# Optimization experiments

Hardware: AMD Instinct MI355X
Metric: run time of the kernel (lower is better)

Reference implementation:

```python
import jax, jax.numpy as jnp
import numpy as np

N, M, C = 4096, 1024, 64
KERNEL_SIZE = (0.1, 0.1)  # box extents; threshold is kernel_size/2 on |dx|,|dy|


def setup_inputs() -> dict:
    key = jax.random.key(0)
    k1, k2, k3 = jax.random.split(key, 3)
    values = jax.random.normal(k1, (N, C), dtype=jnp.float32)
    coords = jax.random.uniform(k2, (N, 2), dtype=jnp.float32)
    query_coords = jax.random.uniform(k3, (M, 2), dtype=jnp.float32)
    return {"values": values, "coords": coords, "query_coords": query_coords}


def reference(values, coords, query_coords):
    # shift buffer is (0,0) so no shift branch; box-kernel mask branch.
    kw, kh = KERNEL_SIZE
    diffs = query_coords[:, None, :] - coords[None, :, :]          # [M, N, 2]
    mask = (jnp.abs(diffs[..., 0]) < kw / 2) & (jnp.abs(diffs[..., 1]) < kh / 2)  # [M, N]
    neg = jnp.finfo(values.dtype).min
    # per-query masked max over points == ragged split + per-segment max in the original
    masked = jnp.where(mask[:, :, None], values[None, :, :], neg)  # [M, N, C]
    return jnp.max(masked, axis=1)                                  # [M, C]
```

## Files before the change

kernel.cpp:

```cpp
#include <hip/hip_runtime.h>

constexpr int N = 4096;
constexpr int M = 1024;
constexpr int C = 64;
#define HALF_KW 0.05f
#define NEG_INF (-3.402823466e38f)

__global__ __launch_bounds__(256) void maxpool_box_kernel(
    const float* __restrict__ values,
    const float* __restrict__ coords,
    const float* __restrict__ qcoords,
    float* __restrict__ out)
{
    __shared__ int    s_cnt;
    __shared__ int    s_list[N];
    __shared__ float4 s_part[16][16];

    const int q    = blockIdx.x;
    const int tid  = threadIdx.x;
    const int lane = tid & 63;
    const int w    = tid >> 6;

    if (tid == 0) s_cnt = 0;
    __syncthreads();

    const float qx = qcoords[2 * q + 0];
    const float qy = qcoords[2 * q + 1];

    const float4* c4p = (const float4*)coords;
    #pragma unroll
    for (int i = 0; i < N / (256 * 2); ++i) {
        const int pair = i * 256 + tid;
        const float4 cc = c4p[pair];
        const bool in0 = (fabsf(qx - cc.x) < HALF_KW) && (fabsf(qy - cc.y) < HALF_KW);
        const bool in1 = (fabsf(qx - cc.z) < HALF_KW) && (fabsf(qy - cc.w) < HALF_KW);
        if (in0) { int k = atomicAdd(&s_cnt, 1); s_list[k] = 2 * pair; }
        if (in1) { int k = atomicAdd(&s_cnt, 1); s_list[k] = 2 * pair + 1; }
    }
    __syncthreads();

    const int cnt = s_cnt;
    const int G   = (cnt + 3) >> 2;
    if (cnt > 0 && tid < G * 4 - cnt) s_list[cnt + tid] = s_list[0];
    __syncthreads();

    const int sub = lane >> 4;
    const int cq  = lane & 15;
    const float4* v4 = (const float4*)values;
    float4 acc = make_float4(NEG_INF, NEG_INF, NEG_INF, NEG_INF);
    for (int g = w; g < G; g += 4) {
        const int p = s_list[g * 4 + sub];
        const float4 v = v4[p * 16 + cq];
        acc.x = fmaxf(acc.x, v.x);
        acc.y = fmaxf(acc.y, v.y);
        acc.z = fmaxf(acc.z, v.z);
        acc.w = fmaxf(acc.w, v.w);
    }
    s_part[w * 4 + sub][cq] = acc;
    __syncthreads();

    if (tid < 16) {
        float4 r = s_part[0][tid];
        #pragma unroll
        for (int k = 1; k < 16; ++k) {
            const float4 t = s_part[k][tid];
            r.x = fmaxf(r.x, t.x);
            r.y = fmaxf(r.y, t.y);
            r.z = fmaxf(r.z, t.z);
            r.w = fmaxf(r.w, t.w);
        }
        ((float4*)out)[q * 16 + tid] = r;
    }
}

extern "C" void kernel_launch(void* const* d_in, const int* in_sizes, int n_in,
                              void* d_out, int out_size, void* d_ws, size_t ws_size,
                              hipStream_t stream) {
    const float* values  = (const float*)d_in[0];
    const float* coords  = (const float*)d_in[1];
    const float* qcoords = (const float*)d_in[2];
    float* out = (float*)d_out;

    maxpool_box_kernel<<<M, 256, 0, stream>>>(values, coords, qcoords, out);
}
```

Baseline: 61.25 us.

## Bin points into a uniform grid so queries scan only nearby cells

```diff
diff --git a/kernel.cpp b/kernel.cpp
--- a/kernel.cpp
+++ b/kernel.cpp
@@ -3,13 +3,73 @@
 constexpr int N = 4096;
 constexpr int M = 1024;
 constexpr int C = 64;
+constexpr int GRID = 20;
+constexpr int NCELL = GRID * GRID;
+#define CELL_INV 20.0f
 #define HALF_KW 0.05f
 #define NEG_INF (-3.402823466e38f)
 
-__global__ __launch_bounds__(256) void maxpool_box_kernel(
+
+__global__ __launch_bounds__(1024) void bin_points_kernel(
+    const float* __restrict__ coords,
+    int* __restrict__ cell_start,
+    int* __restrict__ binned_idx,
+    float2* __restrict__ binned_xy)
+{
+    __shared__ int s_cnt[NCELL];
+    __shared__ int s_scan[512];
+    __shared__ int s_cur[NCELL];
+
+    const int tid = threadIdx.x;
+
+    if (tid < NCELL) s_cnt[tid] = 0;
+    __syncthreads();
+
+    const float4* c4 = (const float4*)coords;
+    const float4 a = c4[2 * tid];
+    const float4 b = c4[2 * tid + 1];
+    const float px[4] = {a.x, a.z, b.x, b.z};
+    const float py[4] = {a.y, a.w, b.y, b.w};
+    int cell[4];
+    #pragma unroll
+    for (int k = 0; k < 4; ++k) {
+        const int cx = min(GRID - 1, (int)(px[k] * CELL_INV));
+        const int cy = min(GRID - 1, (int)(py[k] * CELL_INV));
+        cell[k] = cy * GRID + cx;
+        atomicAdd(&s_cnt[cell[k]], 1);
+    }
+    __syncthreads();
+
+    if (tid < 512) s_scan[tid] = (tid < NCELL) ? s_cnt[tid] : 0;
+    __syncthreads();
+    for (int off = 1; off < 512; off <<= 1) {
+        int v = 0;
+        if (tid < 512) { v = s_scan[tid]; if (tid >= off) v += s_scan[tid - off]; }
+        __syncthreads();
+        if (tid < 512) s_scan[tid] = v;
+        __syncthreads();
+    }
+    if (tid <= NCELL) {
+        const int e = (tid == 0) ? 0 : s_scan[tid - 1];
+        cell_start[tid] = e;
+        if (tid < NCELL) s_cur[tid] = e;
+    }
+    __syncthreads();
+
+    #pragma unroll
+    for (int k = 0; k < 4; ++k) {
+        const int pos = atomicAdd(&s_cur[cell[k]], 1);
+        binned_idx[pos] = 4 * tid + k;
+        binned_xy[pos]  = make_float2(px[k], py[k]);
+    }
+}
+
+__global__ __launch_bounds__(256) void maxpool_query_kernel(
     const float* __restrict__ values,
-    const float* __restrict__ coords,
     const float* __restrict__ qcoords,
+    const int* __restrict__ cell_start,
+    const int* __restrict__ binned_idx,
+    const float2* __restrict__ binned_xy,
     float* __restrict__ out)
 {
     __shared__ int    s_cnt;
@@ -22,20 +82,39 @@
     const int w    = tid >> 6;
 
     if (tid == 0) s_cnt = 0;
-    __syncthreads();
 
     const float qx = qcoords[2 * q + 0];
     const float qy = qcoords[2 * q + 1];
 
-    const float4* c4p = (const float4*)coords;
+    const int cx0 = max(0,        (int)floorf((qx - HALF_KW - 1e-4f) * CELL_INV));
+    const int cx1 = min(GRID - 1, (int)floorf((qx + HALF_KW + 1e-4f) * CELL_INV));
+    const int cy0 = max(0,        (int)floorf((qy - HALF_KW - 1e-4f) * CELL_INV));
+    const int cy1 = min(GRID - 1, (int)floorf((qy + HALF_KW + 1e-4f) * CELL_INV));
+    const int nrows = cy1 - cy0 + 1;
+
+    int base[3], len[3];
     #pragma unroll
-    for (int i = 0; i < N / (256 * 2); ++i) {
-        const int pair = i * 256 + tid;
-        const float4 cc = c4p[pair];
-        const bool in0 = (fabsf(qx - cc.x) < HALF_KW) && (fabsf(qy - cc.y) < HALF_KW);
-        const bool in1 = (fabsf(qx - cc.z) < HALF_KW) && (fabsf(qy - cc.w) < HALF_KW);
-        if (in0) { int k = atomicAdd(&s_cnt, 1); s_list[k] = 2 * pair; }
-        if (in1) { int k = atomicAdd(&s_cnt, 1); s_list[k] = 2 * pair + 1; }
+    for (int r = 0; r < 3; ++r) {
+        if (r < nrows) {
+            const int row = (cy0 + r) * GRID;
+            const int lo = cell_start[row + cx0];
+            const int hi = cell_start[row + cx1 + 1];
+            base[r] = lo; len[r] = hi - lo;
+        } else { base[r] = 0; len[r] = 0; }
+    }
+    const int total = len[0] + len[1] + len[2];
+    __syncthreads();
+
+    for (int t = tid; t < total; t += 256) {
+        int j;
+        if (t < len[0])               j = base[0] + t;
+        else if (t < len[0] + len[1]) j = base[1] + (t - len[0]);
+        else                          j = base[2] + (t - len[0] - len[1]);
+        const float2 cc = binned_xy[j];
+        if (fabsf(qx - cc.x) < HALF_KW && fabsf(qy - cc.y) < HALF_KW) {
+            const int k = atomicAdd(&s_cnt, 1);
+            s_list[k] = binned_idx[j];
+        }
     }
     __syncthreads();
 
@@ -81,5 +160,12 @@
     const float* qcoords = (const float*)d_in[2];
     float* out = (float*)d_out;
 
-    maxpool_box_kernel<<<M, 256, 0, stream>>>(values, coords, qcoords, out);
+    char* ws = (char*)d_ws;
+    int*    cell_start = (int*)(ws + 0);
+    int*    binned_idx = (int*)(ws + 4096);
+    float2* binned_xy  = (float2*)(ws + 20480);
+
+    bin_points_kernel<<<1, 1024, 0, stream>>>(coords, cell_start, binned_idx, binned_xy);
+    maxpool_query_kernel<<<M, 256, 0, stream>>>(values, qcoords, cell_start,
+                                                binned_idx, binned_xy, out);
 }
```

New measurement: 67.60 us. +10.4%, slower.

## Replace shared-memory atomic compaction with wavefront ballot and direct max accumulation

Applied to the files above, without the earlier changes.

```diff
diff --git a/kernel.cpp b/kernel.cpp
--- a/kernel.cpp
+++ b/kernel.cpp
@@ -12,64 +12,45 @@
     const float* __restrict__ qcoords,
     float* __restrict__ out)
 {
-    __shared__ int    s_cnt;
-    __shared__ int    s_list[N];
-    __shared__ float4 s_part[16][16];
+    __shared__ float s_acc[4][64];
 
     const int q    = blockIdx.x;
     const int tid  = threadIdx.x;
     const int lane = tid & 63;
     const int w    = tid >> 6;
 
-    if (tid == 0) s_cnt = 0;
-    __syncthreads();
-
     const float qx = qcoords[2 * q + 0];
     const float qy = qcoords[2 * q + 1];
 
     const float4* c4p = (const float4*)coords;
+    float acc = NEG_INF;
+
     #pragma unroll
-    for (int i = 0; i < N / (256 * 2); ++i) {
-        const int pair = i * 256 + tid;
-        const float4 cc = c4p[pair];
+    for (int it = 0; it < 8; ++it) {
+        const int pairbase = (w << 9) + (it << 6);
+        const float4 cc = c4p[pairbase + lane];
         const bool in0 = (fabsf(qx - cc.x) < HALF_KW) && (fabsf(qy - cc.y) < HALF_KW);
         const bool in1 = (fabsf(qx - cc.z) < HALF_KW) && (fabsf(qy - cc.w) < HALF_KW);
-        if (in0) { int k = atomicAdd(&s_cnt, 1); s_list[k] = 2 * pair; }
-        if (in1) { int k = atomicAdd(&s_cnt, 1); s_list[k] = 2 * pair + 1; }
+        unsigned long long b0 = __ballot(in0);
+        unsigned long long b1 = __ballot(in1);
+        while (b0) {
+            const int i = __builtin_ctzll(b0); b0 &= b0 - 1;
+            const int p = 2 * (pairbase + i);
+            acc = fmaxf(acc, values[p * C + lane]);
+        }
+        while (b1) {
+            const int i = __builtin_ctzll(b1); b1 &= b1 - 1;
+            const int p = 2 * (pairbase + i) + 1;
+            acc = fmaxf(acc, values[p * C + lane]);
+        }
     }
+
+    s_acc[w][lane] = acc;
     __syncthreads();
-
-    const int cnt = s_cnt;
-    const int G   = (cnt + 3) >> 2;
-    if (cnt > 0 && tid < G * 4 - cnt) s_list[cnt + tid] = s_list[0];
-    __syncthreads();
-
-    const int sub = lane >> 4;
-    const int cq  = lane & 15;
-    const float4* v4 = (const float4*)values;
-    float4 acc = make_float4(NEG_INF, NEG_INF, NEG_INF, NEG_INF);
-    for (int g = w; g < G; g += 4) {
-        const int p = s_list[g * 4 + sub];
-        const float4 v = v4[p * 16 + cq];
-        acc.x = fmaxf(acc.x, v.x);
-        acc.y = fmaxf(acc.y, v.y);
-        acc.z = fmaxf(acc.z, v.z);
-        acc.w = fmaxf(acc.w, v.w);
-    }
-    s_part[w * 4 + sub][cq] = acc;
-    __syncthreads();
-
-    if (tid < 16) {
-        float4 r = s_part[0][tid];
-        #pragma unroll
-        for (int k = 1; k < 16; ++k) {
-            const float4 t = s_part[k][tid];
-            r.x = fmaxf(r.x, t.x);
-            r.y = fmaxf(r.y, t.y);
-            r.z = fmaxf(r.z, t.z);
-            r.w = fmaxf(r.w, t.w);
-        }
-        ((float4*)out)[q * 16 + tid] = r;
+    if (tid < 64) {
+        const float r = fmaxf(fmaxf(s_acc[0][tid], s_acc[1][tid]),
+                              fmaxf(s_acc[2][tid], s_acc[3][tid]));
+        out[q * C + tid] = r;
     }
 }
 
```

Measured after the change: 63.00 us. +2.9%, slower.

## Build per-wavefront match lists with ballot compaction instead of shared atomics

Applied to the files above, without the earlier changes.

```diff
diff --git a/kernel.cpp b/kernel.cpp
--- a/kernel.cpp
+++ b/kernel.cpp
@@ -12,8 +12,7 @@
     const float* __restrict__ qcoords,
     float* __restrict__ out)
 {
-    __shared__ int    s_cnt;
-    __shared__ int    s_list[N];
+    __shared__ int    s_list[4][1024];
     __shared__ float4 s_part[16][16];
 
     const int q    = blockIdx.x;
@@ -21,42 +20,44 @@
     const int lane = tid & 63;
     const int w    = tid >> 6;
 
-    if (tid == 0) s_cnt = 0;
-    __syncthreads();
-
-    const float qx = qcoords[2 * q + 0];
-    const float qy = qcoords[2 * q + 1];
+    const float2 qc = ((const float2*)qcoords)[q];
+    const float qx = qc.x, qy = qc.y;
 
     const float4* c4p = (const float4*)coords;
+    int cnt = 0;
     #pragma unroll
-    for (int i = 0; i < N / (256 * 2); ++i) {
-        const int pair = i * 256 + tid;
-        const float4 cc = c4p[pair];
+    for (int it = 0; it < 8; ++it) {
+        const int pairbase = (w << 9) + (it << 6);
+        const float4 cc = c4p[pairbase + lane];
         const bool in0 = (fabsf(qx - cc.x) < HALF_KW) && (fabsf(qy - cc.y) < HALF_KW);
         const bool in1 = (fabsf(qx - cc.z) < HALF_KW) && (fabsf(qy - cc.w) < HALF_KW);
-        if (in0) { int k = atomicAdd(&s_cnt, 1); s_list[k] = 2 * pair; }
-        if (in1) { int k = atomicAdd(&s_cnt, 1); s_list[k] = 2 * pair + 1; }
+        const unsigned long long b0 = __ballot(in0);
+        const unsigned long long b1 = __ballot(in1);
+        int pos0 = __builtin_amdgcn_mbcnt_lo((unsigned)b0, 0);
+        pos0     = __builtin_amdgcn_mbcnt_hi((unsigned)(b0 >> 32), pos0);
+        if (in0) s_list[w][cnt + pos0] = 2 * (pairbase + lane);
+        cnt += __popcll(b0);
+        int pos1 = __builtin_amdgcn_mbcnt_lo((unsigned)b1, 0);
+        pos1     = __builtin_amdgcn_mbcnt_hi((unsigned)(b1 >> 32), pos1);
+        if (in1) s_list[w][cnt + pos1] = 2 * (pairbase + lane) + 1;
+        cnt += __popcll(b1);
     }
-    __syncthreads();
-
-    const int cnt = s_cnt;
-    const int G   = (cnt + 3) >> 2;
-    if (cnt > 0 && tid < G * 4 - cnt) s_list[cnt + tid] = s_list[0];
-    __syncthreads();
 
     const int sub = lane >> 4;
     const int cq  = lane & 15;
     const float4* v4 = (const float4*)values;
     float4 acc = make_float4(NEG_INF, NEG_INF, NEG_INF, NEG_INF);
-    for (int g = w; g < G; g += 4) {
-        const int p = s_list[g * 4 + sub];
+    const int G = (cnt + 3) >> 2;
+    for (int g = 0; g < G; ++g) {
+        const int t = (g << 2) + sub;
+        const int p = s_list[w][t < cnt ? t : 0];
         const float4 v = v4[p * 16 + cq];
         acc.x = fmaxf(acc.x, v.x);
         acc.y = fmaxf(acc.y, v.y);
         acc.z = fmaxf(acc.z, v.z);
         acc.w = fmaxf(acc.w, v.w);
     }
-    s_part[w * 4 + sub][cq] = acc;
+    s_part[(w << 2) + sub][cq] = acc;
     __syncthreads();
 
     if (tid < 16) {
```

After: 61.45 us. Within noise of the previous version (+0.3%).
